# Kernel tuning notes

Measured on AMD Instinct MI355X. Metric: run time of the kernel, lower is better.

Reference implementation:

```python
import jax, jax.numpy as jnp
import numpy as np

HIDDEN = 1024
MOE_INTER = 512
SHARED_INTER = 2048
N_EXPERTS = 32
TOP_K = 6
N_GROUP = 8
TOPK_GROUP = 4
ROUTED_SCALE = 2.5


def setup_inputs() -> dict:
    key = jax.random.key(0)
    ks = jax.random.split(key, 6)
    s = 0.02
    return {
        "hidden_states": jax.random.normal(ks[0], (2, 1024, HIDDEN), jnp.float32),
        "gate_w": jax.random.normal(ks[1], (N_EXPERTS, HIDDEN), jnp.float32) * s,
        "e_bias": jnp.zeros((N_EXPERTS,), jnp.float32),  # e_score_correction_bias (non-trainable)
        "up_w": jax.random.normal(ks[2], (N_EXPERTS, MOE_INTER, HIDDEN), jnp.float32) * s,
        "down_w": jax.random.normal(ks[3], (N_EXPERTS, HIDDEN, MOE_INTER), jnp.float32) * s,
        "shared_up_w": jax.random.normal(ks[4], (SHARED_INTER, HIDDEN), jnp.float32) * s,
        "shared_down_w": jax.random.normal(ks[5], (HIDDEN, SHARED_INTER), jnp.float32) * s,
    }


def _relu2(x):
    # Nemotron-H 'relu2' activation: relu(x)^2
    return jnp.square(jax.nn.relu(x))


def _router(x, gate_w, e_bias):
    # x: [T, H] -> topk_idx [T, K] (int), topk_w [T, K] (fp32)
    T = x.shape[0]
    logits = x.astype(jnp.float32) @ gate_w.astype(jnp.float32).T  # [T, E]
    scores = jax.nn.sigmoid(logits)
    sc = scores + e_bias[None, :]
    # group-limited routing: top-2 sum per group, keep topk_group groups
    g = sc.reshape(T, N_GROUP, N_EXPERTS // N_GROUP)
    group_scores = jax.lax.top_k(g, 2)[0].sum(-1)                  # [T, G]
    group_idx = jax.lax.top_k(group_scores, TOPK_GROUP)[1]         # [T, TG]
    group_mask = jnp.zeros_like(group_scores).at[jnp.arange(T)[:, None], group_idx].set(1.0)
    score_mask = jnp.repeat(group_mask, N_EXPERTS // N_GROUP, axis=1)  # [T, E]
    masked = jnp.where(score_mask > 0, sc, 0.0)
    topk_idx = jax.lax.stop_gradient(jax.lax.top_k(masked, TOP_K)[1])  # torch path is @no_grad
    topk_w = jnp.take_along_axis(scores, topk_idx, axis=1)         # gather from unbiased scores
    topk_w = topk_w / (topk_w.sum(-1, keepdims=True) + 1e-20)      # norm_topk_prob
    topk_w = topk_w * ROUTED_SCALE
    return topk_idx, topk_w


def reference(hidden_states, gate_w, e_bias, up_w, down_w, shared_up_w, shared_down_w):
    B, S, H = hidden_states.shape
    x = hidden_states.reshape(-1, H)  # [T, H]
    T = x.shape[0]
    topk_idx, topk_w = _router(x, gate_w, e_bias)
    # combine weights as dense [T, E] (scatter of top-k weights)
    combine = jnp.zeros((T, N_EXPERTS), topk_w.dtype).at[jnp.arange(T)[:, None], topk_idx].add(topk_w)
    # dense-masked expert compute; weight applied on intermediate (equivalent since
    # down_proj is linear with no bias): out = sum_e w_te * down_e(act(up_e(x)))
    h = _relu2(jnp.einsum('th,eih->tei', x, up_w))   # [T, E, I]
    h = h * combine[:, :, None]
    moe_out = jnp.einsum('tei,ehi->th', h, down_w)   # [T, H]
    shared = _relu2(x @ shared_up_w.T) @ shared_down_w.T
    return (moe_out + shared).reshape(B, S, H)


if __name__ == "__main__":
    out = reference(**setup_inputs())
    print(out.shape, out.dtype)
```

## Files before the change

### kernel.cpp

```cpp
#include <hip/hip_runtime.h>

typedef unsigned short u16;
typedef __bf16 bf16x8 __attribute__((ext_vector_type(8)));
typedef float f32x4 __attribute__((ext_vector_type(4)));
typedef u16 u16x8 __attribute__((ext_vector_type(8)));

#define T_TOK 2048
#define HID   1024
#define NEXP  32
#define IM    512
#define SI    2048
#define TOPK  6
#define PLAN_MAX 160

__device__ __forceinline__ u16 f2bf(float f){
  unsigned u = __float_as_uint(f);
  u += 0x7FFFu + ((u >> 16) & 1u);
  return (u16)(u >> 16);
}

__device__ __forceinline__ void gll16(const void* g, void* l){
  __builtin_amdgcn_global_load_lds((const __attribute__((address_space(1))) void*)g,
                                   (__attribute__((address_space(3))) void*)l, 16, 0, 0);
}

__device__ __forceinline__ u16x8 cvt2(float4 a, float4 b){
  u16x8 o;
  o[0] = f2bf(a.x); o[1] = f2bf(a.y); o[2] = f2bf(a.z); o[3] = f2bf(a.w);
  o[4] = f2bf(b.x); o[5] = f2bf(b.y); o[6] = f2bf(b.z); o[7] = f2bf(b.w);
  return o;
}

__global__ __launch_bounds__(256) void prep_kernel(
    const float* __restrict__ x, const float4* __restrict__ upw, const float4* __restrict__ dnw,
    const float4* __restrict__ supw, const float4* __restrict__ sdnw,
    const float* __restrict__ gate, const float* __restrict__ ebias,
    u16x8* __restrict__ xb, u16x8* __restrict__ upb, u16x8* __restrict__ dnb,
    u16x8* __restrict__ supb, u16x8* __restrict__ sdnb,
    int* __restrict__ ce, float* __restrict__ cw, int* __restrict__ done){
  int blk = blockIdx.x;
  if (blk == 0 && threadIdx.x == 0) *done = 0;
  if (blk >= 512){
    const float4* s; u16x8* d; long i;
    if (blk < 16896){
      i = (long)(blk - 512) * 256 + threadIdx.x;
      if (i < 2097152L){ s = upw; d = upb; }
      else             { s = dnw; d = dnb; i -= 2097152L; }
    } else {
      i = (long)(blk - 16896) * 256 + threadIdx.x;
      if      (i < 262144L){ s = (const float4*)x; d = xb; }
      else if (i < 524288L){ s = supw; d = supb; i -= 262144L; }
      else                 { s = sdnw; d = sdnb; i -= 524288L; }
    }
    float4 a = s[2*i], b = s[2*i+1];
    d[i] = cvt2(a, b);
    return;
  }
  int wave = threadIdx.x >> 6;
  int lane = threadIdx.x & 63;
  int t = blk * 4 + wave;
  int e = lane & 31, half = lane >> 5;
  const float4* xv = (const float4*)(x + (size_t)t * HID);
  const float4* gv = (const float4*)(gate + (size_t)e * HID);
  double d0a = 0, d1a = 0, d2a = 0, d3a = 0;
  for (int i = half * 128; i < half * 128 + 128; i++){
    float4 a = xv[i], b = gv[i];
    d0a += (double)a.x * b.x; d1a += (double)a.y * b.y;
    d2a += (double)a.z * b.z; d3a += (double)a.w * b.w;
  }
  double acc = (d0a + d1a) + (d2a + d3a);
  acc += __shfl_xor(acc, 32);
  double score = 1.0 / (1.0 + exp(-acc));
  double sc = score + (double)ebias[e];
  double o1  = __shfl_xor(sc, 1);
  double hi  = fmax(sc, o1), lo = fmin(sc, o1);
  double ohi = __shfl_xor(hi, 2), olo = __shfl_xor(lo, 2);
  double gs  = (hi >= ohi) ? hi + fmax(lo, ohi) : ohi + fmax(olo, hi);
  int g = e >> 2;
  int rank = 0;
#pragma unroll
  for (int j = 0; j < 8; j++){
    double gj = __shfl(gs, j * 4);
    if (gj > gs || (gj == gs && j < g)) rank++;
  }
  double cur = (rank < 4) ? sc : 0.0;
  int sel_e[TOPK]; double sel_w[TOPK]; double wsum = 0.0;
#pragma unroll
  for (int k = 0; k < TOPK; k++){
    double bv = cur; int bi = lane;
#pragma unroll
    for (int m = 32; m >= 1; m >>= 1){
      double ov = __shfl_xor(bv, m); int oi = __shfl_xor(bi, m);
      if (ov > bv || (ov == bv && oi < bi)) { bv = ov; bi = oi; }
    }
    if ((bi & 31) == e) cur = -1e300;
    double ws = __shfl(score, bi);
    sel_e[k] = bi; sel_w[k] = ws; wsum += ws;
  }
  double scale = 2.5 / (wsum + 1e-20);
#pragma unroll
  for (int k = 0; k < TOPK; k++){
    if (lane == k){
      ce[t * TOPK + k] = sel_e[k] & 31;
      cw[t * TOPK + k] = (float)(sel_w[k] * scale);
    }
  }
}

__global__ __launch_bounds__(256) void build_plan_kernel(const int* __restrict__ ce,
                                                         const float* __restrict__ cw,
                                                         int* __restrict__ cnt,
                                                         int* __restrict__ tok,
                                                         float* __restrict__ wl,
                                                         int* __restrict__ done,
                                                         int* __restrict__ plan){
  int e = blockIdx.x;
  int tid = threadIdx.x, lane = tid & 63, wave = tid >> 6;
  __shared__ int wsum[4];
  __shared__ int lastflag;
  int running = 0;
  for (int base = 0; base < T_TOK * TOPK; base += 256){
    int i = base + tid;
    bool m = (ce[i] == e);
    unsigned long long bal = __ballot(m);
    int woff = __popcll(bal & ((1ull << lane) - 1ull));
    if (lane == 0) wsum[wave] = __popcll(bal);
    __syncthreads();
    int wbase = 0;
#pragma unroll
    for (int wv = 0; wv < 4; wv++) if (wv < wave) wbase += wsum[wv];
    int btot = wsum[0] + wsum[1] + wsum[2] + wsum[3];
    if (m){
      int t = i / TOPK, k = i - t * TOPK;
      int pos = running + wbase + woff;
      tok[e * T_TOK + pos] = (t << 3) | k;
      wl[e * T_TOK + pos] = cw[i];
    }
    running += btot;
    __syncthreads();
  }
  if (tid == 0){
    atomicExch(&cnt[e], running);
    __threadfence();
    lastflag = (atomicAdd(done, 1) == NEXP - 1);
  }
  __syncthreads();
  if (lastflag){
    __threadfence();
    if (tid < PLAN_MAX) plan[1 + tid] = -1;
    __syncthreads();
    if (tid == 0){
      int n = 0;
      for (int ee = 0; ee < NEXP; ee++){
        int c = (ee == e) ? running : cnt[ee];
        for (int tb = 0; tb < c; tb += 128) plan[1 + n++] = (tb << 8) | ee;
      }
      plan[0] = n;
    }
  }
}

__device__ __forceinline__ void gemm_core(
    const char* gA0, const char* gA1, const char* gB0, const char* gB1,
    u16* lA, u16* lB, int iters, int tid, int wrow, int wcol, int qsw, int l16,
    f32x4 acc[4][4])
{
  char* bA = (char*)lA + tid*16;
  char* bB = (char*)lB + tid*16;
  gll16(gA0, bA);  gll16(gA1, bA + 4096);
  gll16(gB0, bB);  gll16(gB1, bB + 4096);
  gA0 += 64; gA1 += 64; gB0 += 64; gB1 += 64;
  __syncthreads();
  unsigned cur = 0;
  for (int it = 0; it < iters - 1; ++it){
    unsigned nxt = cur ^ 1;
    gll16(gA0, bA + nxt*8192);  gll16(gA1, bA + nxt*8192 + 4096);
    gll16(gB0, bB + nxt*8192);  gll16(gB1, bB + nxt*8192 + 4096);
    gA0 += 64; gA1 += 64; gB0 += 64; gB1 += 64;
    const u16* rA = lA + cur*4096;
    const u16* rB = lB + cur*4096;
    bf16x8 af[4], bfr[4];
#pragma unroll
    for (int mt = 0; mt < 4; mt++) af[mt]  = *(const bf16x8*)&rA[(wrow + mt*16 + l16)*32 + qsw*8];
#pragma unroll
    for (int nt = 0; nt < 4; nt++) bfr[nt] = *(const bf16x8*)&rB[(wcol + nt*16 + l16)*32 + qsw*8];
#pragma unroll
    for (int mt = 0; mt < 4; mt++)
#pragma unroll
      for (int nt = 0; nt < 4; nt++)
        acc[mt][nt] = __builtin_amdgcn_mfma_f32_16x16x32_bf16(af[mt], bfr[nt], acc[mt][nt], 0, 0, 0);
    __syncthreads();
    cur = nxt;
  }
  const u16* rA = lA + cur*4096;
  const u16* rB = lB + cur*4096;
  bf16x8 af[4], bfr[4];
#pragma unroll
  for (int mt = 0; mt < 4; mt++) af[mt]  = *(const bf16x8*)&rA[(wrow + mt*16 + l16)*32 + qsw*8];
#pragma unroll
  for (int nt = 0; nt < 4; nt++) bfr[nt] = *(const bf16x8*)&rB[(wcol + nt*16 + l16)*32 + qsw*8];
#pragma unroll
  for (int mt = 0; mt < 4; mt++)
#pragma unroll
    for (int nt = 0; nt < 4; nt++)
      acc[mt][nt] = __builtin_amdgcn_mfma_f32_16x16x32_bf16(af[mt], bfr[nt], acc[mt][nt], 0, 0, 0);
}

#define ACC_INIT f32x4 acc[4][4]; \
  _Pragma("unroll") for (int i_ = 0; i_ < 4; i_++) \
  _Pragma("unroll") for (int j_ = 0; j_ < 4; j_++) acc[i_][j_] = (f32x4){0.f,0.f,0.f,0.f};

#define GEO_INIT int tid = threadIdx.x; \
  int lane = tid & 63, wave = tid >> 6, quad = lane >> 4, l16 = lane & 15; \
  int wrow = (wave >> 1)*64, wcol = (wave & 1)*64; \
  int srow = tid >> 2; \
  int sseg = ((tid & 3) ^ ((tid >> 3) & 3)) * 16; \
  int qsw  = quad ^ ((l16 >> 1) & 3);

__global__ __launch_bounds__(256) void up_fused_kernel(
    const u16* __restrict__ xb, const u16* __restrict__ supb, const u16* __restrict__ upb,
    const int* __restrict__ cnt, const int* __restrict__ tok, const float* __restrict__ wl,
    const int* __restrict__ plan, u16* __restrict__ shh, u16* __restrict__ hws){
  __shared__ u16 lA[2*128*32], lB[2*128*32];
  GEO_INIT;
  int blk = blockIdx.x;
  if (blk < 256){
    int bm = (blk >> 4) * 128, bn = (blk & 15) * 128;
    const char* gA0 = (const char*)(xb + (size_t)(bm + srow)*HID) + sseg;
    const char* gA1 = (const char*)(xb + (size_t)(bm + 64 + srow)*HID) + sseg;
    const char* gB0 = (const char*)(supb + (size_t)(bn + srow)*HID) + sseg;
    const char* gB1 = (const char*)(supb + (size_t)(bn + 64 + srow)*HID) + sseg;
    ACC_INIT;
    gemm_core(gA0, gA1, gB0, gB1, lA, lB, HID/32, tid, wrow, wcol, qsw, l16, acc);
#pragma unroll
    for (int mt = 0; mt < 4; mt++)
#pragma unroll
      for (int nt = 0; nt < 4; nt++)
#pragma unroll
        for (int r = 0; r < 4; r++){
          int m = bm + wrow + mt*16 + quad*4 + r;
          int n = bn + wcol + nt*16 + l16;
          float v = acc[mt][nt][r]; v = fmaxf(v, 0.f); v *= v;
          shh[(size_t)m*SI + n] = f2bf(v);
        }
  } else {
    int eu = blk - 256;
    int pv = plan[1 + (eu >> 2)];
    if (pv < 0) return;
    int e = pv & 255;
    int tb = pv >> 8;
    int c = cnt[e];
    int bn = (eu & 3) * 128;
    const int* tl = tok + e * T_TOK;
    const float* wle = wl + e * T_TOK;
    int s0 = tb + srow;      if (s0 > c-1) s0 = c-1;
    int s1 = tb + 64 + srow; if (s1 > c-1) s1 = c-1;
    int t0 = tl[s0] >> 3, t1 = tl[s1] >> 3;
    const char* gA0 = (const char*)(xb + (size_t)t0*HID) + sseg;
    const char* gA1 = (const char*)(xb + (size_t)t1*HID) + sseg;
    const u16* Bb = upb + (size_t)e * IM * HID;
    const char* gB0 = (const char*)(Bb + (size_t)(bn + srow)*HID) + sseg;
    const char* gB1 = (const char*)(Bb + (size_t)(bn + 64 + srow)*HID) + sseg;
    ACC_INIT;
    gemm_core(gA0, gA1, gB0, gB1, lA, lB, HID/32, tid, wrow, wcol, qsw, l16, acc);
#pragma unroll
    for (int mt = 0; mt < 4; mt++)
#pragma unroll
      for (int r = 0; r < 4; r++){
        int s = tb + wrow + mt*16 + quad*4 + r;
        if (s < c){
          int code = tl[s];
          float w = wle[s];
          size_t hb = ((size_t)(code >> 3) * TOPK + (code & 7)) * IM;
#pragma unroll
          for (int nt = 0; nt < 4; nt++){
            float v = acc[mt][nt][r]; v = fmaxf(v, 0.f); v = v * v * w;
            hws[hb + bn + wcol + nt*16 + l16] = f2bf(v);
          }
        }
      }
  }
}

__global__ __launch_bounds__(256) void down_fused_kernel(
    const u16* __restrict__ shh, const u16* __restrict__ sdnb,
    const u16* __restrict__ hws, const u16* __restrict__ dnb,
    const int* __restrict__ cnt, const int* __restrict__ tok, const int* __restrict__ plan,
    float* __restrict__ out){
  __shared__ u16 lA[2*128*32], lB[2*128*32];
  GEO_INIT;
  int blk = blockIdx.x;
  if (blk < 512){
    int kc = blk & 3;
    int bn = ((blk >> 2) & 7) * 128;
    int bm = (blk >> 5) * 128;
    const char* gA0 = (const char*)(shh + (size_t)(bm + srow)*SI + kc*512) + sseg;
    const char* gA1 = (const char*)(shh + (size_t)(bm + 64 + srow)*SI + kc*512) + sseg;
    const char* gB0 = (const char*)(sdnb + (size_t)(bn + srow)*SI + kc*512) + sseg;
    const char* gB1 = (const char*)(sdnb + (size_t)(bn + 64 + srow)*SI + kc*512) + sseg;
    ACC_INIT;
    gemm_core(gA0, gA1, gB0, gB1, lA, lB, 16, tid, wrow, wcol, qsw, l16, acc);
#pragma unroll
    for (int mt = 0; mt < 4; mt++)
#pragma unroll
      for (int nt = 0; nt < 4; nt++)
#pragma unroll
        for (int r = 0; r < 4; r++){
          int m = bm + wrow + mt*16 + quad*4 + r;
          int n = bn + wcol + nt*16 + l16;
          unsafeAtomicAdd(&out[(size_t)m*HID + n], acc[mt][nt][r]);
        }
  } else {
    int eu = blk - 512;
    int pv = plan[1 + (eu >> 3)];
    if (pv < 0) return;
    int e = pv & 255;
    int tb = pv >> 8;
    int c = cnt[e];
    int bn = (eu & 7) * 128;
    const int* tl = tok + e * T_TOK;
    int s0 = tb + srow;      if (s0 > c-1) s0 = c-1;
    int s1 = tb + 64 + srow; if (s1 > c-1) s1 = c-1;
    int c0 = tl[s0], c1 = tl[s1];
    const char* gA0 = (const char*)(hws + ((size_t)(c0 >> 3)*TOPK + (c0 & 7))*IM) + sseg;
    const char* gA1 = (const char*)(hws + ((size_t)(c1 >> 3)*TOPK + (c1 & 7))*IM) + sseg;
    const u16* Bb = dnb + (size_t)e * HID * IM;
    const char* gB0 = (const char*)(Bb + (size_t)(bn + srow)*IM) + sseg;
    const char* gB1 = (const char*)(Bb + (size_t)(bn + 64 + srow)*IM) + sseg;
    ACC_INIT;
    gemm_core(gA0, gA1, gB0, gB1, lA, lB, IM/32, tid, wrow, wcol, qsw, l16, acc);
#pragma unroll
    for (int mt = 0; mt < 4; mt++)
#pragma unroll
      for (int r = 0; r < 4; r++){
        int s = tb + wrow + mt*16 + quad*4 + r;
        if (s < c){
          int code = tl[s];
          float* ob = out + (size_t)(code >> 3) * HID;
#pragma unroll
          for (int nt = 0; nt < 4; nt++)
            unsafeAtomicAdd(&ob[bn + wcol + nt*16 + l16], acc[mt][nt][r]);
        }
      }
  }
}

extern "C" void kernel_launch(void* const* d_in, const int* in_sizes, int n_in,
                              void* d_out, int out_size, void* d_ws, size_t ws_size,
                              hipStream_t stream) {
  const float* x    = (const float*)d_in[0];
  const float* gate = (const float*)d_in[1];
  const float* eb   = (const float*)d_in[2];
  const float* upw  = (const float*)d_in[3];
  const float* dnw  = (const float*)d_in[4];
  const float* supw = (const float*)d_in[5];
  const float* sdnw = (const float*)d_in[6];
  float* out = (float*)d_out;

  char* w = (char*)d_ws;
  size_t o = 0;
  int*   cnt  = (int*)(w + o);   o += 1024;
  int*   plan = (int*)(w + o);   o += 1024;
  int*   ce   = (int*)(w + o);   o += (size_t)T_TOK * TOPK * 4;
  float* cw   = (float*)(w + o); o += (size_t)T_TOK * TOPK * 4;
  int*   tok  = (int*)(w + o);   o += (size_t)NEXP * T_TOK * 4;
  float* wl   = (float*)(w + o); o += (size_t)NEXP * T_TOK * 4;
  u16*   xb   = (u16*)(w + o);   o += (size_t)T_TOK * HID * 2;
  u16*   dnb  = (u16*)(w + o);   o += (size_t)NEXP * HID * IM * 2;
  u16*   hws  = (u16*)(w + o);   o += (size_t)T_TOK * TOPK * IM * 2;
  u16*   upb  = (u16*)(w + o);   o += (size_t)NEXP * IM * HID * 2;
  u16*   supb = (u16*)(w + o);   o += (size_t)SI * HID * 2;
  u16*   sdnb = (u16*)(w + o);   o += (size_t)HID * SI * 2;
  u16*   shh  = (u16*)(w + o);   o += (size_t)T_TOK * SI * 2;
  int*   done = cnt + 32;

  hipMemsetAsync(out, 0, (size_t)T_TOK * HID * 4, stream);
  prep_kernel<<<19968, 256, 0, stream>>>(
      x, (const float4*)upw, (const float4*)dnw, (const float4*)supw, (const float4*)sdnw,
      gate, eb, (u16x8*)xb, (u16x8*)upb, (u16x8*)dnb, (u16x8*)supb, (u16x8*)sdnb,
      ce, cw, done);
  build_plan_kernel<<<NEXP, 256, 0, stream>>>(ce, cw, cnt, tok, wl, done, plan);
  up_fused_kernel<<<896, 256, 0, stream>>>(xb, supb, upb, cnt, tok, wl, plan, shh, hws);
  down_fused_kernel<<<1792, 256, 0, stream>>>(shh, sdnb, hws, dnb, cnt, tok, plan, out);
}
```

Measured before the change: 360.0 us.

## Triple-buffer GEMM LDS pipeline and drop split-K for shared down projection

Replaces the double-buffered global-to-LDS GEMM loop with a three-stage ring that keeps two tiles in flight, using explicit vmcnt waits and raw barriers. The goal is to hide global load latency behind MFMA work. The shared-expert down projection also drops its 4-way split-K: 128 blocks now run the full K=2048 instead of 512 blocks each doing a quarter. This cuts atomic-add traffic to the output, but the shared part gets fewer, longer blocks and LDS use per block rises by half, which may lower occupancy.

```diff
diff --git a/kernel.cpp b/kernel.cpp
--- a/kernel.cpp
+++ b/kernel.cpp
@@ -160,50 +160,61 @@
   }
 }
 
-__device__ __forceinline__ void gemm_core(
+__device__ __forceinline__ void gemm_pipe(
     const char* gA0, const char* gA1, const char* gB0, const char* gB1,
     u16* lA, u16* lB, int iters, int tid, int wrow, int wcol, int qsw, int l16,
     f32x4 acc[4][4])
 {
   char* bA = (char*)lA + tid*16;
   char* bB = (char*)lB + tid*16;
-  gll16(gA0, bA);  gll16(gA1, bA + 4096);
-  gll16(gB0, bB);  gll16(gB1, bB + 4096);
-  gA0 += 64; gA1 += 64; gB0 += 64; gB1 += 64;
-  __syncthreads();
-  unsigned cur = 0;
-  for (int it = 0; it < iters - 1; ++it){
-    unsigned nxt = cur ^ 1;
-    gll16(gA0, bA + nxt*8192);  gll16(gA1, bA + nxt*8192 + 4096);
-    gll16(gB0, bB + nxt*8192);  gll16(gB1, bB + nxt*8192 + 4096);
-    gA0 += 64; gA1 += 64; gB0 += 64; gB1 += 64;
-    const u16* rA = lA + cur*4096;
-    const u16* rB = lB + cur*4096;
-    bf16x8 af[4], bfr[4];
-#pragma unroll
-    for (int mt = 0; mt < 4; mt++) af[mt]  = *(const bf16x8*)&rA[(wrow + mt*16 + l16)*32 + qsw*8];
-#pragma unroll
-    for (int nt = 0; nt < 4; nt++) bfr[nt] = *(const bf16x8*)&rB[(wcol + nt*16 + l16)*32 + qsw*8];
-#pragma unroll
-    for (int mt = 0; mt < 4; mt++)
-#pragma unroll
-      for (int nt = 0; nt < 4; nt++)
-        acc[mt][nt] = __builtin_amdgcn_mfma_f32_16x16x32_bf16(af[mt], bfr[nt], acc[mt][nt], 0, 0, 0);
-    __syncthreads();
-    cur = nxt;
-  }
-  const u16* rA = lA + cur*4096;
-  const u16* rB = lB + cur*4096;
-  bf16x8 af[4], bfr[4];
-#pragma unroll
-  for (int mt = 0; mt < 4; mt++) af[mt]  = *(const bf16x8*)&rA[(wrow + mt*16 + l16)*32 + qsw*8];
-#pragma unroll
-  for (int nt = 0; nt < 4; nt++) bfr[nt] = *(const bf16x8*)&rB[(wcol + nt*16 + l16)*32 + qsw*8];
-#pragma unroll
-  for (int mt = 0; mt < 4; mt++)
-#pragma unroll
-    for (int nt = 0; nt < 4; nt++)
-      acc[mt][nt] = __builtin_amdgcn_mfma_f32_16x16x32_bf16(af[mt], bfr[nt], acc[mt][nt], 0, 0, 0);
+#define STAGE(t, b) do { \
+    gll16(gA0 + (size_t)(t)*64, bA + (b)*8192); \
+    gll16(gA1 + (size_t)(t)*64, bA + (b)*8192 + 4096); \
+    gll16(gB0 + (size_t)(t)*64, bB + (b)*8192); \
+    gll16(gB1 + (size_t)(t)*64, bB + (b)*8192 + 4096); } while(0)
+#define COMPUTE(rbuf) do { \
+    const u16* rA = lA + (rbuf)*4096; \
+    const u16* rB = lB + (rbuf)*4096; \
+    bf16x8 af[4], bfr[4]; \
+    _Pragma("unroll") \
+    for (int mt = 0; mt < 4; mt++) af[mt]  = *(const bf16x8*)&rA[(wrow + mt*16 + l16)*32 + qsw*8]; \
+    _Pragma("unroll") \
+    for (int nt = 0; nt < 4; nt++) bfr[nt] = *(const bf16x8*)&rB[(wcol + nt*16 + l16)*32 + qsw*8]; \
+    _Pragma("unroll") \
+    for (int mt = 0; mt < 4; mt++) \
+    _Pragma("unroll") \
+      for (int nt = 0; nt < 4; nt++) \
+        acc[mt][nt] = __builtin_amdgcn_mfma_f32_16x16x32_bf16(af[mt], bfr[nt], acc[mt][nt], 0, 0, 0); \
+    } while(0)
+
+  STAGE(0, 0); STAGE(1, 1);
+  int rb = 0, sb = 2;
+  for (int it = 0; it < iters - 2; ++it){
+    STAGE(it + 2, sb);
+    asm volatile("s_waitcnt vmcnt(8)" ::: "memory");
+    __builtin_amdgcn_s_barrier();
+    asm volatile("" ::: "memory");
+    COMPUTE(rb);
+    asm volatile("" ::: "memory");
+    __builtin_amdgcn_s_barrier();
+    asm volatile("" ::: "memory");
+    rb = (rb + 1 == 3) ? 0 : rb + 1;
+    sb = (sb + 1 == 3) ? 0 : sb + 1;
+  }
+  asm volatile("s_waitcnt vmcnt(4)" ::: "memory");
+  __builtin_amdgcn_s_barrier();
+  asm volatile("" ::: "memory");
+  COMPUTE(rb);
+  asm volatile("" ::: "memory");
+  __builtin_amdgcn_s_barrier();
+  asm volatile("" ::: "memory");
+  rb = (rb + 1 == 3) ? 0 : rb + 1;
+  asm volatile("s_waitcnt vmcnt(0)" ::: "memory");
+  __builtin_amdgcn_s_barrier();
+  asm volatile("" ::: "memory");
+  COMPUTE(rb);
+#undef STAGE
+#undef COMPUTE
 }
 
 #define ACC_INIT f32x4 acc[4][4]; \
@@ -221,7 +232,7 @@
     const u16* __restrict__ xb, const u16* __restrict__ supb, const u16* __restrict__ upb,
     const int* __restrict__ cnt, const int* __restrict__ tok, const float* __restrict__ wl,
     const int* __restrict__ plan, u16* __restrict__ shh, u16* __restrict__ hws){
-  __shared__ u16 lA[2*128*32], lB[2*128*32];
+  __shared__ u16 lA[3*4096], lB[3*4096];
   GEO_INIT;
   int blk = blockIdx.x;
   if (blk < 256){
@@ -231,7 +242,7 @@
     const char* gB0 = (const char*)(supb + (size_t)(bn + srow)*HID) + sseg;
     const char* gB1 = (const char*)(supb + (size_t)(bn + 64 + srow)*HID) + sseg;
     ACC_INIT;
-    gemm_core(gA0, gA1, gB0, gB1, lA, lB, HID/32, tid, wrow, wcol, qsw, l16, acc);
+    gemm_pipe(gA0, gA1, gB0, gB1, lA, lB, HID/32, tid, wrow, wcol, qsw, l16, acc);
 #pragma unroll
     for (int mt = 0; mt < 4; mt++)
 #pragma unroll
@@ -262,7 +273,7 @@
     const char* gB0 = (const char*)(Bb + (size_t)(bn + srow)*HID) + sseg;
     const char* gB1 = (const char*)(Bb + (size_t)(bn + 64 + srow)*HID) + sseg;
     ACC_INIT;
-    gemm_core(gA0, gA1, gB0, gB1, lA, lB, HID/32, tid, wrow, wcol, qsw, l16, acc);
+    gemm_pipe(gA0, gA1, gB0, gB1, lA, lB, HID/32, tid, wrow, wcol, qsw, l16, acc);
 #pragma unroll
     for (int mt = 0; mt < 4; mt++)
 #pragma unroll
@@ -287,19 +298,17 @@
     const u16* __restrict__ hws, const u16* __restrict__ dnb,
     const int* __restrict__ cnt, const int* __restrict__ tok, const int* __restrict__ plan,
     float* __restrict__ out){
-  __shared__ u16 lA[2*128*32], lB[2*128*32];
+  __shared__ u16 lA[3*4096], lB[3*4096];
   GEO_INIT;
   int blk = blockIdx.x;
-  if (blk < 512){
-    int kc = blk & 3;
-    int bn = ((blk >> 2) & 7) * 128;
-    int bm = (blk >> 5) * 128;
-    const char* gA0 = (const char*)(shh + (size_t)(bm + srow)*SI + kc*512) + sseg;
-    const char* gA1 = (const char*)(shh + (size_t)(bm + 64 + srow)*SI + kc*512) + sseg;
-    const char* gB0 = (const char*)(sdnb + (size_t)(bn + srow)*SI + kc*512) + sseg;
-    const char* gB1 = (const char*)(sdnb + (size_t)(bn + 64 + srow)*SI + kc*512) + sseg;
+  if (blk < 128){
+    int bm = (blk >> 3)*128, bn = (blk & 7)*128;
+    const char* gA0 = (const char*)(shh + (size_t)(bm + srow)*SI) + sseg;
+    const char* gA1 = (const char*)(shh + (size_t)(bm + 64 + srow)*SI) + sseg;
+    const char* gB0 = (const char*)(sdnb + (size_t)(bn + srow)*SI) + sseg;
+    const char* gB1 = (const char*)(sdnb + (size_t)(bn + 64 + srow)*SI) + sseg;
     ACC_INIT;
-    gemm_core(gA0, gA1, gB0, gB1, lA, lB, 16, tid, wrow, wcol, qsw, l16, acc);
+    gemm_pipe(gA0, gA1, gB0, gB1, lA, lB, SI/32, tid, wrow, wcol, qsw, l16, acc);
 #pragma unroll
     for (int mt = 0; mt < 4; mt++)
 #pragma unroll
@@ -311,7 +320,7 @@
           unsafeAtomicAdd(&out[(size_t)m*HID + n], acc[mt][nt][r]);
         }
   } else {
-    int eu = blk - 512;
+    int eu = blk - 128;
     int pv = plan[1 + (eu >> 3)];
     if (pv < 0) return;
     int e = pv & 255;
@@ -328,7 +337,7 @@
     const char* gB0 = (const char*)(Bb + (size_t)(bn + srow)*IM) + sseg;
     const char* gB1 = (const char*)(Bb + (size_t)(bn + 64 + srow)*IM) + sseg;
     ACC_INIT;
-    gemm_core(gA0, gA1, gB0, gB1, lA, lB, IM/32, tid, wrow, wcol, qsw, l16, acc);
+    gemm_pipe(gA0, gA1, gB0, gB1, lA, lB, IM/32, tid, wrow, wcol, qsw, l16, acc);
 #pragma unroll
     for (int mt = 0; mt < 4; mt++)
 #pragma unroll
@@ -381,5 +390,5 @@
       ce, cw, done);
   build_plan_kernel<<<NEXP, 256, 0, stream>>>(ce, cw, cnt, tok, wl, done, plan);
   up_fused_kernel<<<896, 256, 0, stream>>>(xb, supb, upb, cnt, tok, wl, plan, shh, hws);
-  down_fused_kernel<<<1792, 256, 0, stream>>>(shh, sdnb, hws, dnb, cnt, tok, plan, out);
-}
+  down_fused_kernel<<<1408, 256, 0, stream>>>(shh, sdnb, hws, dnb, cnt, tok, plan, out);
+}
```

New measurement: 335.7 us. -6.8%, faster.
